# Performance work log

Measured on AMD Instinct MI355X. Metric: run time of the kernel, lower is better.

Reference implementation:

```python
import jax, jax.numpy as jnp
import numpy as np

B, N, C, NH = 4, 2304, 256, 8
HD = C // NH            # head dim = 32
HS = WS = 48            # H = W = sqrt(N)
RADIUS = 3.0
MLP_HID = 4 * C
SCALE = HD ** (-0.5)
NEG = -1e9              # stands in for -inf (identical softmax up to fp eps)
EPS = 1e-6


def spatial_mask():
    # get_spatial_mask: cdist of (y, x) grid coords, -inf where dist > radius
    yy, xx = jnp.meshgrid(jnp.arange(HS), jnp.arange(WS), indexing='ij')
    coords = jnp.stack([yy, xx], -1).reshape(-1, 2).astype(jnp.float32)  # [N, 2]
    d2 = jnp.sum((coords[:, None, :] - coords[None, :, :]) ** 2, -1)     # [N, N]
    return jnp.where(d2 > RADIUS * RADIUS, NEG, 0.0)


def layernorm(x, g, b):
    mu = jnp.mean(x, -1, keepdims=True)
    var = jnp.mean((x - mu) ** 2, -1, keepdims=True)
    return (x - mu) * jax.lax.rsqrt(var + EPS) * g + b


def setup_inputs() -> dict:
    key = jax.random.key(0)
    ks = jax.random.split(key, 16)
    s = 0.02
    return {
        'x':    jax.random.normal(ks[0], (B, N, C), jnp.float32),
        'x_kv': jax.random.normal(ks[1], (B, N, C), jnp.float32),
        'Wq': jax.random.normal(ks[2], (C, C), jnp.float32) * s,
        'bq': jnp.zeros((C,), jnp.float32),
        'Wk': jax.random.normal(ks[3], (C, C), jnp.float32) * s,
        'bk': jnp.zeros((C,), jnp.float32),
        'Wv': jax.random.normal(ks[4], (C, C), jnp.float32) * s,
        'bv': jnp.zeros((C,), jnp.float32),
        'Wp': jax.random.normal(ks[5], (C, C), jnp.float32) * s,
        'bp': jnp.zeros((C,), jnp.float32),
        'g1': jnp.ones((C,), jnp.float32),
        'b1': jnp.zeros((C,), jnp.float32),
        'g2': jnp.ones((C,), jnp.float32),
        'b2': jnp.zeros((C,), jnp.float32),
        'W1': jax.random.normal(ks[6], (C, MLP_HID), jnp.float32) * s,
        'bm1': jnp.zeros((MLP_HID,), jnp.float32),
        'W2': jax.random.normal(ks[7], (MLP_HID, C), jnp.float32) * s,
        'bm2': jnp.zeros((C,), jnp.float32),
    }


def reference(x, x_kv, Wq, bq, Wk, bk, Wv, bv, Wp, bp,
              g1, b1, g2, b2, W1, bm1, W2, bm2):
    mask = spatial_mask()                                  # [N, N]
    h = layernorm(x, g1, b1)
    hkv = layernorm(x_kv, g1, b1)
    q = (h @ Wq + bq).reshape(B, N, NH, HD)
    k = (hkv @ Wk + bk).reshape(B, N, NH, HD)
    v = (hkv @ Wv + bv).reshape(B, N, NH, HD)
    scores = jnp.einsum('bqhd,bkhd->bhqk', q, k) * SCALE + mask
    attn = jax.nn.softmax(scores, axis=-1)
    out = jnp.einsum('bhqk,bkhd->bqhd', attn, v).reshape(B, N, C)
    x = x + out @ Wp + bp
    m = layernorm(x, g2, b2)
    x = x + jax.nn.gelu(m @ W1 + bm1, approximate=False) @ W2 + bm2
    return x
```

## Files before the change

kernel.cpp:

```cpp
#include <hip/hip_runtime.h>
#include <hip/hip_fp16.h>
#include <math.h>

#define BB 4
#define NN 2304
#define CC 256
#define HS 48
#define HID 1024
#define BNROWS (BB * NN)
#define ATTN_SCALE 0.17677669529663687f

typedef _Float16 f16;
typedef __attribute__((ext_vector_type(2))) _Float16 h2;
typedef __attribute__((ext_vector_type(8))) _Float16 h8;
typedef __attribute__((ext_vector_type(4))) float f4;

#define GLLS16(g, l)                                                        \
    __builtin_amdgcn_global_load_lds(                                       \
        (const __attribute__((address_space(1))) unsigned int*)(g),         \
        (__attribute__((address_space(3))) unsigned int*)(l), 16, 0, 0)

#define WAIT_VM0()   asm volatile("s_waitcnt vmcnt(0)" ::: "memory")
#define WAIT_LGKM0() asm volatile("s_waitcnt lgkmcnt(0)" ::: "memory")

static __device__ __forceinline__ float wave_sum64(float v) {
    v += __shfl_xor(v, 32, 64);
    v += __shfl_xor(v, 16, 64);
    v += __shfl_xor(v, 8, 64);
    v += __shfl_xor(v, 4, 64);
    v += __shfl_xor(v, 2, 64);
    v += __shfl_xor(v, 1, 64);
    return v;
}

__global__ __launch_bounds__(256) void prep_kernel(
    const float* __restrict__ Wq, const float* __restrict__ Wk,
    const float* __restrict__ Wv, const float* __restrict__ Wp,
    const float* __restrict__ W1, const float* __restrict__ W2,
    const float* __restrict__ bq, const float* __restrict__ bk,
    const float* __restrict__ bv,
    f16* __restrict__ WqkvT, f16* __restrict__ WpT,
    f16* __restrict__ W1T, f16* __restrict__ W2T, float* __restrict__ bqkv)
{
    int bx = blockIdx.x;
    if (bx == 768) {
        const int t = threadIdx.x;
        bqkv[t]       = bq[t];
        bqkv[t + 256] = bk[t];
        bqkv[t + 512] = bv[t];
        return;
    }
    __shared__ float tt[32][33];
    const float* src; f16* dst; int K, N;
    if (bx < 64)        { src = Wq; dst = WqkvT;             K = 256;  N = 256; }
    else if (bx < 128)  { src = Wk; dst = WqkvT + 65536;     K = 256;  N = 256;  bx -= 64; }
    else if (bx < 192)  { src = Wv; dst = WqkvT + 131072;    K = 256;  N = 256;  bx -= 128; }
    else if (bx < 256)  { src = Wp; dst = WpT;               K = 256;  N = 256;  bx -= 192; }
    else if (bx < 512)  { src = W1; dst = W1T;               K = 256;  N = 1024; bx -= 256; }
    else                { src = W2; dst = W2T;               K = 1024; N = 256;  bx -= 512; }
    const int tN = N >> 5;
    const int kt = bx / tN, nt = bx - kt * tN;
    const int rr = threadIdx.x >> 5, cc = threadIdx.x & 31;
#pragma unroll
    for (int j = 0; j < 4; ++j)
        tt[rr + 8 * j][cc] = src[(size_t)(kt * 32 + rr + 8 * j) * N + nt * 32 + cc];
    __syncthreads();
#pragma unroll
    for (int j = 0; j < 4; ++j)
        dst[(size_t)(nt * 32 + rr + 8 * j) * K + kt * 32 + cc] = (f16)tt[cc][rr + 8 * j];
}

__global__ __launch_bounds__(256) void ln1_kernel(
    const float* __restrict__ x, const float* __restrict__ xkv,
    const float* __restrict__ g, const float* __restrict__ be,
    f16* __restrict__ hq, f16* __restrict__ hkv)
{
    const int r = blockIdx.x * 4 + (threadIdx.x >> 6);
    const int lane = threadIdx.x & 63;
    const float* src; f16* dst;
    if (r < BNROWS) { src = x + (size_t)r * CC;             dst = hq + (size_t)r * CC; }
    else { src = xkv + (size_t)(r - BNROWS) * CC; dst = hkv + (size_t)(r - BNROWS) * CC; }
    const float4 v = ((const float4*)src)[lane];
    const float mu = wave_sum64(v.x + v.y + v.z + v.w) * (1.0f / CC);
    const float d0 = v.x - mu, d1 = v.y - mu, d2 = v.z - mu, d3 = v.w - mu;
    const float var = wave_sum64(d0 * d0 + d1 * d1 + d2 * d2 + d3 * d3) * (1.0f / CC);
    const float rs = rsqrtf(var + 1e-6f);
    const float4 g4 = ((const float4*)g)[lane];
    const float4 b4 = ((const float4*)be)[lane];
    h2 o01 = (h2){(f16)(d0 * rs * g4.x + b4.x), (f16)(d1 * rs * g4.y + b4.y)};
    h2 o23 = (h2){(f16)(d2 * rs * g4.z + b4.z), (f16)(d3 * rs * g4.w + b4.w)};
    ((h2*)dst)[lane * 2] = o01;
    ((h2*)dst)[lane * 2 + 1] = o23;
}

__global__ __launch_bounds__(256) void ln2_kernel(
    const f16* __restrict__ x1, const float* __restrict__ g,
    const float* __restrict__ be, f16* __restrict__ m2)
{
    const int r = blockIdx.x * 4 + (threadIdx.x >> 6);
    const int lane = threadIdx.x & 63;
    const f16* src = x1 + (size_t)r * CC;
    const h2 a01 = ((const h2*)src)[lane * 2];
    const h2 a23 = ((const h2*)src)[lane * 2 + 1];
    const float v0 = (float)a01[0], v1 = (float)a01[1];
    const float v2 = (float)a23[0], v3 = (float)a23[1];
    const float mu = wave_sum64(v0 + v1 + v2 + v3) * (1.0f / CC);
    const float d0 = v0 - mu, d1 = v1 - mu, d2 = v2 - mu, d3 = v3 - mu;
    const float var = wave_sum64(d0 * d0 + d1 * d1 + d2 * d2 + d3 * d3) * (1.0f / CC);
    const float rs = rsqrtf(var + 1e-6f);
    const float4 g4 = ((const float4*)g)[lane];
    const float4 b4 = ((const float4*)be)[lane];
    f16* dst = m2 + (size_t)r * CC;
    h2 o01 = (h2){(f16)(d0 * rs * g4.x + b4.x), (f16)(d1 * rs * g4.y + b4.y)};
    h2 o23 = (h2){(f16)(d2 * rs * g4.z + b4.z), (f16)(d3 * rs * g4.w + b4.w)};
    ((h2*)dst)[lane * 2] = o01;
    ((h2*)dst)[lane * 2 + 1] = o23;
}

template <int TM, bool GELU, int RESID, bool OUTF32, bool QKV>
__global__ __launch_bounds__(256, 4) void gemm_wave(
    const f16* __restrict__ Aq, const f16* __restrict__ Akv,
    const f16* __restrict__ Bt, const float* __restrict__ bias,
    const void* __restrict__ resid, void* __restrict__ out1,
    void* __restrict__ outkv, int M, int N, int K)
{
    constexpr int AT = TM / 16;
    constexpr int AELEM = TM * 32;
    __shared__ f16 lds[4 * (AELEM + 2048)];
    const int tid = threadIdx.x;
    const int wid = tid >> 6, lane = tid & 63;
    const int ln15 = lane & 15, quad = lane >> 4;
    f16* Al = lds + wid * (AELEM + 2048);
    f16* Bl = Al + AELEM;
    const int n0 = blockIdx.x * 64;
    const int m0 = (blockIdx.y * 4 + wid) * TM;
    const f16* Ap = QKV ? (n0 < 256 ? Aq : Akv) : Aq;

    const int jr = lane >> 2, js = lane & 3;
    size_t ga[AT], gb[4];
#pragma unroll
    for (int i = 0; i < AT; ++i) {
        const int r = i * 16 + jr;
        const int q = (js - (r >> 1)) & 3;
        ga[i] = (size_t)(m0 + r) * K + q * 8;
    }
#pragma unroll
    for (int i = 0; i < 4; ++i) {
        const int r = i * 16 + jr;
        const int q = (js - (r >> 1)) & 3;
        gb[i] = (size_t)(n0 + r) * K + q * 8;
    }
    int aoff[AT], boff[4];
#pragma unroll
    for (int mt = 0; mt < AT; ++mt) {
        const int r = mt * 16 + ln15;
        aoff[mt] = (r * 4 + ((quad + (r >> 1)) & 3)) * 16;
    }
#pragma unroll
    for (int nt = 0; nt < 4; ++nt) {
        const int r = nt * 16 + ln15;
        boff[nt] = (r * 4 + ((quad + (r >> 1)) & 3)) * 16;
    }

    f4 acc[AT][4];
#pragma unroll
    for (int i = 0; i < AT; ++i)
#pragma unroll
        for (int j = 0; j < 4; ++j) acc[i][j] = (f4){0.f, 0.f, 0.f, 0.f};

    for (int k0 = 0; k0 < K; k0 += 32) {
        if (k0) WAIT_LGKM0();
#pragma unroll
        for (int i = 0; i < AT; ++i)
            GLLS16(Ap + ga[i] + k0, Al + i * 512);
#pragma unroll
        for (int i = 0; i < 4; ++i)
            GLLS16(Bt + gb[i] + k0, Bl + i * 512);
        WAIT_VM0();
        h8 bF[4], aF[AT];
#pragma unroll
        for (int nt = 0; nt < 4; ++nt)
            bF[nt] = *(const h8*)((const char*)Bl + boff[nt]);
#pragma unroll
        for (int mt = 0; mt < AT; ++mt)
            aF[mt] = *(const h8*)((const char*)Al + aoff[mt]);
#pragma unroll
        for (int mt = 0; mt < AT; ++mt)
#pragma unroll
            for (int nt = 0; nt < 4; ++nt)
                acc[mt][nt] = __builtin_amdgcn_mfma_f32_16x16x32_f16(
                    aF[mt], bF[nt], acc[mt][nt], 0, 0, 0);
    }

#pragma unroll
    for (int nt = 0; nt < 4; ++nt) {
        const int gn = n0 + nt * 16 + ln15;
        const float bs = bias[gn];
#pragma unroll
        for (int mt = 0; mt < AT; ++mt) {
#pragma unroll
            for (int r = 0; r < 4; ++r) {
                const int gm = m0 + mt * 16 + quad * 4 + r;
                float v = acc[mt][nt][r] + bs;
                if (GELU) v = 0.5f * v * (1.0f + erff(v * 0.70710678118654752f));
                if (RESID == 1) v += ((const float*)resid)[(size_t)gm * N + gn];
                if (RESID == 2) v += (float)((const f16*)resid)[(size_t)gm * N + gn];
                if (QKV) {
                    if (gn < 256) ((f16*)out1)[(size_t)gm * 256 + gn] = (f16)v;
                    else ((f16*)outkv)[(size_t)gm * 512 + (gn - 256)] = (f16)v;
                } else if (OUTF32) {
                    ((float*)out1)[(size_t)gm * N + gn] = v;
                } else {
                    ((f16*)out1)[(size_t)gm * N + gn] = (f16)v;
                }
            }
        }
    }
}

__device__ __constant__ int ATT_DY[29] = {
    -3, -2, -2, -2, -2, -2, -1, -1, -1, -1, -1, 0, 0, 0, 0,
    0, 0, 0, 1, 1, 1, 1, 1, 2, 2, 2, 2, 2, 3};
__device__ __constant__ int ATT_DX[29] = {
    0, -2, -1, 0, 1, 2, -2, -1, 0, 1, 2, -3, -2, -1, 0,
    1, 2, 3, -2, -1, 0, 1, 2, -2, -1, 0, 1, 2, 0};

__global__ __launch_bounds__(128) void attn_tile_kernel(
    const f16* __restrict__ qf, const f16* __restrict__ kvf,
    f16* __restrict__ ao)
{
    __shared__ f16 ks[196][66];
    __shared__ f16 vs[196][66];
    const int tile = blockIdx.x, hp = blockIdx.y, b = blockIdx.z;
    const int ty0 = (tile / 6) * 8, tx0 = (tile - (tile / 6) * 6) * 8;
    const int tid = threadIdx.x;

    for (int idx = tid; idx < 196 * 16; idx += 128) {
        const int r = idx >> 4, seg = idx & 15;
        const int gy = ty0 - 3 + r / 14, gx = tx0 - 3 + (r - (r / 14) * 14);
        uint4 val = {0u, 0u, 0u, 0u};
        if ((unsigned)gy < HS && (unsigned)gx < HS) {
            const size_t rowb = ((size_t)b * NN + gy * HS + gx) * 512;
            const int ch = (seg < 8) ? (hp * 64 + seg * 8)
                                     : (256 + hp * 64 + (seg - 8) * 8);
            val = *(const uint4*)&kvf[rowb + ch];
        }
        f16* dstp = (seg < 8) ? &ks[r][(seg & 7) * 8] : &vs[r][(seg & 7) * 8];
        ((unsigned int*)dstp)[0] = val.x;
        ((unsigned int*)dstp)[1] = val.y;
        ((unsigned int*)dstp)[2] = val.z;
        ((unsigned int*)dstp)[3] = val.w;
    }
    __syncthreads();

    const int q = tid & 63, hh = tid >> 6;
    const int qy = q >> 3, qx = q & 7;
    const size_t qrow = (size_t)b * NN + (ty0 + qy) * HS + tx0 + qx;
    const f16* qp = qf + qrow * CC + hp * 64 + hh * 32;
    uint4 qa[4];
#pragma unroll
    for (int i = 0; i < 4; ++i) qa[i] = ((const uint4*)qp)[i];
    const h2* q2 = (const h2*)qa;

    float s[29];
#pragma unroll
    for (int n = 0; n < 29; ++n) {
        const int dy = ATT_DY[n], dx = ATT_DX[n];
        const int r = (qy + 3 + dy) * 14 + qx + 3 + dx;
        const bool valid = (unsigned)(ty0 + qy + dy) < HS &&
                           (unsigned)(tx0 + qx + dx) < HS;
        float a = 0.0f;
        const h2* kp = (const h2*)&ks[r][hh * 32];
#pragma unroll
        for (int i = 0; i < 16; ++i)
            a = __builtin_amdgcn_fdot2(q2[i], kp[i], a, false);
        s[n] = valid ? a * ATTN_SCALE : -1e30f;
    }
    float m = s[0];
#pragma unroll
    for (int n = 1; n < 29; ++n) m = fmaxf(m, s[n]);
    float l = 0.0f;
#pragma unroll
    for (int n = 0; n < 29; ++n) { s[n] = __expf(s[n] - m); l += s[n]; }
    h2 a2[16];
#pragma unroll
    for (int i = 0; i < 16; ++i) a2[i] = (h2){(f16)0.f, (f16)0.f};
#pragma unroll
    for (int n = 0; n < 29; ++n) {
        const int dy = ATT_DY[n], dx = ATT_DX[n];
        const int r = (qy + 3 + dy) * 14 + qx + 3 + dx;
        const f16 pn = (f16)s[n];
        const h2 ph = (h2){pn, pn};
        const h2* vp = (const h2*)&vs[r][hh * 32];
#pragma unroll
        for (int i = 0; i < 16; ++i) a2[i] += ph * vp[i];
    }
    const float inv = 1.0f / l;
    uint4 ov[4];
    f16* oh = (f16*)ov;
#pragma unroll
    for (int i = 0; i < 16; ++i) {
        oh[2 * i]     = (f16)((float)a2[i][0] * inv);
        oh[2 * i + 1] = (f16)((float)a2[i][1] * inv);
    }
    uint4* dst = (uint4*)(ao + qrow * CC + hp * 64 + hh * 32);
#pragma unroll
    for (int i = 0; i < 4; ++i) dst[i] = ov[i];
}

extern "C" void kernel_launch(void* const* d_in, const int* in_sizes, int n_in,
                              void* d_out, int out_size, void* d_ws, size_t ws_size,
                              hipStream_t stream) {
    const float* x    = (const float*)d_in[0];
    const float* x_kv = (const float*)d_in[1];
    const float* Wq   = (const float*)d_in[2];
    const float* bq   = (const float*)d_in[3];
    const float* Wk   = (const float*)d_in[4];
    const float* bk   = (const float*)d_in[5];
    const float* Wv   = (const float*)d_in[6];
    const float* bv   = (const float*)d_in[7];
    const float* Wp   = (const float*)d_in[8];
    const float* bp   = (const float*)d_in[9];
    const float* g1   = (const float*)d_in[10];
    const float* b1   = (const float*)d_in[11];
    const float* g2   = (const float*)d_in[12];
    const float* b2   = (const float*)d_in[13];
    const float* W1   = (const float*)d_in[14];
    const float* bm1  = (const float*)d_in[15];
    const float* W2   = (const float*)d_in[16];
    const float* bm2  = (const float*)d_in[17];
    float* outp = (float*)d_out;

    f16* wsh = (f16*)d_ws;
    f16* WqkvT = wsh;
    f16* WpT   = wsh + 196608;
    f16* W1T   = wsh + 262144;
    f16* W2T   = wsh + 524288;
    float* bqkv = (float*)(wsh + 786432);
    f16* hq    = wsh + 787968;
    f16* hkv   = wsh + 3147264;
    f16* qf    = wsh + 5506560;
    f16* kvf   = wsh + 7865856;
    f16* ao    = hq;
    f16* x1    = hkv;
    f16* m2    = qf;
    f16* hidF  = kvf;
    const bool fused = ws_size >= (size_t)17303040 * sizeof(f16);

    prep_kernel<<<769, 256, 0, stream>>>(Wq, Wk, Wv, Wp, W1, W2, bq, bk, bv,
                                         WqkvT, WpT, W1T, W2T, bqkv);
    ln1_kernel<<<2 * BNROWS / 4, 256, 0, stream>>>(x, x_kv, g1, b1, hq, hkv);
    gemm_wave<64, false, 0, false, true><<<dim3(12, 36), 256, 0, stream>>>(
        hq, hkv, WqkvT, bqkv, nullptr, qf, kvf, BNROWS, 768, CC);
    attn_tile_kernel<<<dim3(36, 4, BB), 128, 0, stream>>>(qf, kvf, ao);
    gemm_wave<32, false, 1, false, false><<<dim3(4, 72), 256, 0, stream>>>(
        ao, nullptr, WpT, bp, x, x1, nullptr, BNROWS, CC, CC);
    ln2_kernel<<<BNROWS / 4, 256, 0, stream>>>(x1, g2, b2, m2);
    if (fused) {
        gemm_wave<64, true, 0, false, false><<<dim3(16, 36), 256, 0, stream>>>(
            m2, nullptr, W1T, bm1, nullptr, hidF, nullptr, BNROWS, HID, CC);
        gemm_wave<32, false, 2, true, false><<<dim3(4, 72), 256, 0, stream>>>(
            hidF, nullptr, W2T, bm2, x1, outp, nullptr, BNROWS, CC, HID);
    } else {
        for (int b = 0; b < BB; ++b) {
            const size_t off = (size_t)b * NN * CC;
            gemm_wave<64, true, 0, false, false><<<dim3(16, 9), 256, 0, stream>>>(
                m2 + off, nullptr, W1T, bm1, nullptr, hidF, nullptr, NN, HID, CC);
            gemm_wave<32, false, 2, true, false><<<dim3(4, 18), 256, 0, stream>>>(
                hidF, nullptr, W2T, bm2, x1 + off, outp + off, nullptr, NN, CC, HID);
        }
    }
    (void)in_sizes; (void)n_in; (void)out_size;
}
```

Measured before the change: 196.9 us.

## Double-buffer GEMM loads, fix TM=32 tiles, fuse weight prep with LN1

The wave GEMM now double-buffers its per-wave LDS slot. It issues the async global-to-LDS loads for the next K-step before computing on the current one and waits with vmcnt(6), so load latency can overlap the MFMAs. The M tile is fixed at 32 rows per wave for every GEMM, which doubles the grid for the QKV and W1 GEMMs and adds parallelism but lowers per-wave reuse. The weight transpose/prep kernel and LN1 are merged into one launch to save a kernel launch and a dependency gap.

After: 195.9 us. About the same (-0.5%).

```diff
diff --git a/kernel.cpp b/kernel.cpp
--- a/kernel.cpp
+++ b/kernel.cpp
@@ -19,8 +19,8 @@
     __builtin_amdgcn_global_load_lds(                                       \
         (const __attribute__((address_space(1))) unsigned int*)(g),         \
         (__attribute__((address_space(3))) unsigned int*)(l), 16, 0, 0)
-
 #define WAIT_VM0()   asm volatile("s_waitcnt vmcnt(0)" ::: "memory")
+#define WAIT_VM6()   asm volatile("s_waitcnt vmcnt(6)" ::: "memory")
 #define WAIT_LGKM0() asm volatile("s_waitcnt lgkmcnt(0)" ::: "memory")
 
 static __device__ __forceinline__ float wave_sum64(float v) {
@@ -33,52 +33,53 @@
     return v;
 }
 
-__global__ __launch_bounds__(256) void prep_kernel(
+__global__ __launch_bounds__(256) void prep_ln1_kernel(
+    const float* __restrict__ x, const float* __restrict__ xkv,
     const float* __restrict__ Wq, const float* __restrict__ Wk,
     const float* __restrict__ Wv, const float* __restrict__ Wp,
     const float* __restrict__ W1, const float* __restrict__ W2,
     const float* __restrict__ bq, const float* __restrict__ bk,
     const float* __restrict__ bv,
+    const float* __restrict__ g, const float* __restrict__ be,
     f16* __restrict__ WqkvT, f16* __restrict__ WpT,
-    f16* __restrict__ W1T, f16* __restrict__ W2T, float* __restrict__ bqkv)
-{
-    int bx = blockIdx.x;
-    if (bx == 768) {
-        const int t = threadIdx.x;
-        bqkv[t]       = bq[t];
-        bqkv[t + 256] = bk[t];
-        bqkv[t + 512] = bv[t];
-        return;
-    }
-    __shared__ float tt[32][33];
-    const float* src; f16* dst; int K, N;
-    if (bx < 64)        { src = Wq; dst = WqkvT;             K = 256;  N = 256; }
-    else if (bx < 128)  { src = Wk; dst = WqkvT + 65536;     K = 256;  N = 256;  bx -= 64; }
-    else if (bx < 192)  { src = Wv; dst = WqkvT + 131072;    K = 256;  N = 256;  bx -= 128; }
-    else if (bx < 256)  { src = Wp; dst = WpT;               K = 256;  N = 256;  bx -= 192; }
-    else if (bx < 512)  { src = W1; dst = W1T;               K = 256;  N = 1024; bx -= 256; }
-    else                { src = W2; dst = W2T;               K = 1024; N = 256;  bx -= 512; }
-    const int tN = N >> 5;
-    const int kt = bx / tN, nt = bx - kt * tN;
-    const int rr = threadIdx.x >> 5, cc = threadIdx.x & 31;
-#pragma unroll
-    for (int j = 0; j < 4; ++j)
-        tt[rr + 8 * j][cc] = src[(size_t)(kt * 32 + rr + 8 * j) * N + nt * 32 + cc];
-    __syncthreads();
-#pragma unroll
-    for (int j = 0; j < 4; ++j)
-        dst[(size_t)(nt * 32 + rr + 8 * j) * K + kt * 32 + cc] = (f16)tt[cc][rr + 8 * j];
-}
-
-__global__ __launch_bounds__(256) void ln1_kernel(
-    const float* __restrict__ x, const float* __restrict__ xkv,
-    const float* __restrict__ g, const float* __restrict__ be,
+    f16* __restrict__ W1T, f16* __restrict__ W2T, float* __restrict__ bqkv,
     f16* __restrict__ hq, f16* __restrict__ hkv)
 {
-    const int r = blockIdx.x * 4 + (threadIdx.x >> 6);
-    const int lane = threadIdx.x & 63;
+    __shared__ float tt[32][33];
+    int bx = blockIdx.x;
+    const int tid = threadIdx.x;
+    if (bx < 768) {
+        const float* src; f16* dst; int K, N;
+        if (bx < 64)        { src = Wq; dst = WqkvT;           K = 256;  N = 256; }
+        else if (bx < 128)  { src = Wk; dst = WqkvT + 65536;   K = 256;  N = 256;  bx -= 64; }
+        else if (bx < 192)  { src = Wv; dst = WqkvT + 131072;  K = 256;  N = 256;  bx -= 128; }
+        else if (bx < 256)  { src = Wp; dst = WpT;             K = 256;  N = 256;  bx -= 192; }
+        else if (bx < 512)  { src = W1; dst = W1T;             K = 256;  N = 1024; bx -= 256; }
+        else                { src = W2; dst = W2T;             K = 1024; N = 256;  bx -= 512; }
+        const int tN = N >> 5;
+        const int kt = bx / tN, nt = bx - kt * tN;
+        const int rr = tid >> 5, cc = tid & 31;
+#pragma unroll
+        for (int j = 0; j < 4; ++j)
+            tt[rr + 8 * j][cc] = src[(size_t)(kt * 32 + rr + 8 * j) * N + nt * 32 + cc];
+        __syncthreads();
+#pragma unroll
+        for (int j = 0; j < 4; ++j)
+            dst[(size_t)(nt * 32 + rr + 8 * j) * K + kt * 32 + cc] = (f16)tt[cc][rr + 8 * j];
+        return;
+    }
+    if (bx == 768) {
+        if (tid < 256) {
+            bqkv[tid]       = bq[tid];
+            bqkv[tid + 256] = bk[tid];
+            bqkv[tid + 512] = bv[tid];
+        }
+        return;
+    }
+    const int r = (bx - 769) * 4 + (tid >> 6);
+    const int lane = tid & 63;
     const float* src; f16* dst;
-    if (r < BNROWS) { src = x + (size_t)r * CC;             dst = hq + (size_t)r * CC; }
+    if (r < BNROWS) { src = x + (size_t)r * CC;              dst = hq + (size_t)r * CC; }
     else { src = xkv + (size_t)(r - BNROWS) * CC; dst = hkv + (size_t)(r - BNROWS) * CC; }
     const float4 v = ((const float4*)src)[lane];
     const float mu = wave_sum64(v.x + v.y + v.z + v.w) * (1.0f / CC);
@@ -117,29 +118,26 @@
     ((h2*)dst)[lane * 2 + 1] = o23;
 }
 
-template <int TM, bool GELU, int RESID, bool OUTF32, bool QKV>
+template <bool GELU, int RESID, bool OUTF32, bool QKV>
 __global__ __launch_bounds__(256, 4) void gemm_wave(
     const f16* __restrict__ Aq, const f16* __restrict__ Akv,
     const f16* __restrict__ Bt, const float* __restrict__ bias,
     const void* __restrict__ resid, void* __restrict__ out1,
-    void* __restrict__ outkv, int M, int N, int K)
+    void* __restrict__ outkv, int N, int K)
 {
-    constexpr int AT = TM / 16;
-    constexpr int AELEM = TM * 32;
-    __shared__ f16 lds[4 * (AELEM + 2048)];
+    __shared__ f16 lds[4 * 6144];
     const int tid = threadIdx.x;
     const int wid = tid >> 6, lane = tid & 63;
     const int ln15 = lane & 15, quad = lane >> 4;
-    f16* Al = lds + wid * (AELEM + 2048);
-    f16* Bl = Al + AELEM;
+    const int jr = lane >> 2, js = lane & 3;
+    f16* slot = lds + wid * 6144;
     const int n0 = blockIdx.x * 64;
-    const int m0 = (blockIdx.y * 4 + wid) * TM;
+    const int m0 = (blockIdx.y * 4 + wid) * 32;
     const f16* Ap = QKV ? (n0 < 256 ? Aq : Akv) : Aq;
 
-    const int jr = lane >> 2, js = lane & 3;
-    size_t ga[AT], gb[4];
-#pragma unroll
-    for (int i = 0; i < AT; ++i) {
+    size_t ga[2], gb[4];
+#pragma unroll
+    for (int i = 0; i < 2; ++i) {
         const int r = i * 16 + jr;
         const int q = (js - (r >> 1)) & 3;
         ga[i] = (size_t)(m0 + r) * K + q * 8;
@@ -150,9 +148,9 @@
         const int q = (js - (r >> 1)) & 3;
         gb[i] = (size_t)(n0 + r) * K + q * 8;
     }
-    int aoff[AT], boff[4];
-#pragma unroll
-    for (int mt = 0; mt < AT; ++mt) {
+    int aoff[2], boff[4];
+#pragma unroll
+    for (int mt = 0; mt < 2; ++mt) {
         const int r = mt * 16 + ln15;
         aoff[mt] = (r * 4 + ((quad + (r >> 1)) & 3)) * 16;
     }
@@ -162,34 +160,52 @@
         boff[nt] = (r * 4 + ((quad + (r >> 1)) & 3)) * 16;
     }
 
-    f4 acc[AT][4];
-#pragma unroll
-    for (int i = 0; i < AT; ++i)
+    f4 acc[2][4];
+#pragma unroll
+    for (int i = 0; i < 2; ++i)
 #pragma unroll
         for (int j = 0; j < 4; ++j) acc[i][j] = (f4){0.f, 0.f, 0.f, 0.f};
 
+    {
+        f16* Al = slot;
+        f16* Bl = slot + 1024;
+#pragma unroll
+        for (int i = 0; i < 2; ++i) GLLS16(Ap + ga[i], Al + i * 512);
+#pragma unroll
+        for (int i = 0; i < 4; ++i) GLLS16(Bt + gb[i], Bl + i * 512);
+    }
+
+    int cur = 0;
     for (int k0 = 0; k0 < K; k0 += 32) {
-        if (k0) WAIT_LGKM0();
-#pragma unroll
-        for (int i = 0; i < AT; ++i)
-            GLLS16(Ap + ga[i] + k0, Al + i * 512);
-#pragma unroll
-        for (int i = 0; i < 4; ++i)
-            GLLS16(Bt + gb[i] + k0, Bl + i * 512);
-        WAIT_VM0();
-        h8 bF[4], aF[AT];
+        const bool more = (k0 + 32 < K);
+        f16* Ac = slot + cur * 3072;
+        f16* Bc = Ac + 1024;
+        if (more) {
+            f16* An = slot + (cur ^ 1) * 3072;
+            f16* Bn = An + 1024;
+            WAIT_LGKM0();
+#pragma unroll
+            for (int i = 0; i < 2; ++i) GLLS16(Ap + ga[i] + k0 + 32, An + i * 512);
+#pragma unroll
+            for (int i = 0; i < 4; ++i) GLLS16(Bt + gb[i] + k0 + 32, Bn + i * 512);
+            WAIT_VM6();
+        } else {
+            WAIT_VM0();
+        }
+        h8 aF[2], bF[4];
 #pragma unroll
         for (int nt = 0; nt < 4; ++nt)
-            bF[nt] = *(const h8*)((const char*)Bl + boff[nt]);
-#pragma unroll
-        for (int mt = 0; mt < AT; ++mt)
-            aF[mt] = *(const h8*)((const char*)Al + aoff[mt]);
-#pragma unroll
-        for (int mt = 0; mt < AT; ++mt)
+            bF[nt] = *(const h8*)((const char*)Bc + boff[nt]);
+#pragma unroll
+        for (int mt = 0; mt < 2; ++mt)
+            aF[mt] = *(const h8*)((const char*)Ac + aoff[mt]);
+#pragma unroll
+        for (int mt = 0; mt < 2; ++mt)
 #pragma unroll
             for (int nt = 0; nt < 4; ++nt)
                 acc[mt][nt] = __builtin_amdgcn_mfma_f32_16x16x32_f16(
                     aF[mt], bF[nt], acc[mt][nt], 0, 0, 0);
+        cur ^= 1;
     }
 
 #pragma unroll
@@ -197,7 +213,7 @@
         const int gn = n0 + nt * 16 + ln15;
         const float bs = bias[gn];
 #pragma unroll
-        for (int mt = 0; mt < AT; ++mt) {
+        for (int mt = 0; mt < 2; ++mt) {
 #pragma unroll
             for (int r = 0; r < 4; ++r) {
                 const int gm = m0 + mt * 16 + quad * 4 + r;
@@ -347,27 +363,27 @@
     f16* hidF  = kvf;
     const bool fused = ws_size >= (size_t)17303040 * sizeof(f16);
 
-    prep_kernel<<<769, 256, 0, stream>>>(Wq, Wk, Wv, Wp, W1, W2, bq, bk, bv,
-                                         WqkvT, WpT, W1T, W2T, bqkv);
-    ln1_kernel<<<2 * BNROWS / 4, 256, 0, stream>>>(x, x_kv, g1, b1, hq, hkv);
-    gemm_wave<64, false, 0, false, true><<<dim3(12, 36), 256, 0, stream>>>(
-        hq, hkv, WqkvT, bqkv, nullptr, qf, kvf, BNROWS, 768, CC);
+    prep_ln1_kernel<<<5377, 256, 0, stream>>>(
+        x, x_kv, Wq, Wk, Wv, Wp, W1, W2, bq, bk, bv, g1, b1,
+        WqkvT, WpT, W1T, W2T, bqkv, hq, hkv);
+    gemm_wave<false, 0, false, true><<<dim3(12, 72), 256, 0, stream>>>(
+        hq, hkv, WqkvT, bqkv, nullptr, qf, kvf, 768, 256);
     attn_tile_kernel<<<dim3(36, 4, BB), 128, 0, stream>>>(qf, kvf, ao);
-    gemm_wave<32, false, 1, false, false><<<dim3(4, 72), 256, 0, stream>>>(
-        ao, nullptr, WpT, bp, x, x1, nullptr, BNROWS, CC, CC);
+    gemm_wave<false, 1, false, false><<<dim3(4, 72), 256, 0, stream>>>(
+        ao, nullptr, WpT, bp, x, x1, nullptr, 256, 256);
     ln2_kernel<<<BNROWS / 4, 256, 0, stream>>>(x1, g2, b2, m2);
     if (fused) {
-        gemm_wave<64, true, 0, false, false><<<dim3(16, 36), 256, 0, stream>>>(
-            m2, nullptr, W1T, bm1, nullptr, hidF, nullptr, BNROWS, HID, CC);
-        gemm_wave<32, false, 2, true, false><<<dim3(4, 72), 256, 0, stream>>>(
-            hidF, nullptr, W2T, bm2, x1, outp, nullptr, BNROWS, CC, HID);
+        gemm_wave<true, 0, false, false><<<dim3(16, 72), 256, 0, stream>>>(
+            m2, nullptr, W1T, bm1, nullptr, hidF, nullptr, 1024, 256);
+        gemm_wave<false, 2, true, false><<<dim3(4, 72), 256, 0, stream>>>(
+            hidF, nullptr, W2T, bm2, x1, outp, nullptr, 256, 1024);
     } else {
         for (int b = 0; b < BB; ++b) {
             const size_t off = (size_t)b * NN * CC;
-            gemm_wave<64, true, 0, false, false><<<dim3(16, 9), 256, 0, stream>>>(
-                m2 + off, nullptr, W1T, bm1, nullptr, hidF, nullptr, NN, HID, CC);
-            gemm_wave<32, false, 2, true, false><<<dim3(4, 18), 256, 0, stream>>>(
-                hidF, nullptr, W2T, bm2, x1 + off, outp + off, nullptr, NN, CC, HID);
+            gemm_wave<true, 0, false, false><<<dim3(16, 18), 256, 0, stream>>>(
+                m2 + off, nullptr, W1T, bm1, nullptr, hidF, nullptr, 1024, 256);
+            gemm_wave<false, 2, true, false><<<dim3(4, 18), 256, 0, stream>>>(
+                hidF, nullptr, W2T, bm2, x1 + off, outp + off, nullptr, 256, 1024);
         }
     }
     (void)in_sizes; (void)n_in; (void)out_size;
```
